# Performance work log

Hardware: AMD Instinct MI355X
Metric: run time of the kernel (lower is better)

Reference implementation:

```python
import jax, jax.numpy as jnp
import numpy as np

ITERATIONS = 3


def squash(s):
    # Faithful to the torch code: norm is taken over axis 2 (the labels axis
    # for s_j of shape (B, 1, L, O)), exactly as torch's squash(dim=2) does.
    mag_sq = jnp.sum(s * s, axis=2, keepdims=True)
    mag = jnp.sqrt(mag_sq)
    return mag_sq / (1.0 + mag_sq) * (s / mag)


def setup_inputs() -> dict:
    key = jax.random.key(0)
    kx, kw = jax.random.split(key)
    B, N, P, L, O = 256, 8, 1152, 10, 16
    x = jax.random.normal(kx, (B, N, P), dtype=jnp.float32)
    # nn.Parameter(torch.randn(1, P, L, O, N))
    W = jax.random.normal(kw, (1, P, L, O, N), dtype=jnp.float32)
    return {"x": x, "W": W}


def reference(x, W):
    # x: (B, N, P), W: (1, P, L, O, N)
    _, P, L, O, N = W.shape
    u = jnp.transpose(x, (0, 2, 1))  # (B, P, N)
    # u_hat[b,p,l,o] = sum_n W[0,p,l,o,n] * u[b,p,n]
    u_hat = jnp.einsum('plon,bpn->bplo', W[0], u)  # (B, P, L, O)

    b_ij = jnp.zeros((1, P, L, 1), dtype=u_hat.dtype)
    v_j = None
    for _ in range(ITERATIONS):
        # softmax over a size-1 trailing axis -> all ones (faithful to source)
        c_ij = jax.nn.softmax(b_ij, axis=-1)           # (1, P, L, 1)
        s_j = jnp.sum(c_ij * u_hat, axis=1, keepdims=True)  # (B, 1, L, O)
        v_j = squash(s_j)                               # (B, 1, L, O)
        # agreement: <u_hat, v_j> over output dim, then mean over batch
        agree = jnp.einsum('bplo,blo->bpl', u_hat, v_j[:, 0])  # (B, P, L)
        b_ij = b_ij + jnp.mean(agree, axis=0)[None, :, :, None]
    return jnp.squeeze(v_j)  # (B, L, O)
```

## Files before the change

### kernel.cpp

```cpp
#include <hip/hip_runtime.h>
#include <math.h>

#define B_TOT 256
#define N_N   8
#define P_P   1152
#define J_J   160
#define K_K   9216
#define L_L   10

#define SG 18
#define JG 5

typedef __attribute__((ext_vector_type(8))) short short8;
typedef __attribute__((ext_vector_type(4))) float f32x4;

__device__ __forceinline__ short f2bf(float f) {
    unsigned u = __builtin_bit_cast(unsigned, f);
    unsigned r = (u + 0x7fffu + ((u >> 16) & 1u)) >> 16;
    return (short)r;
}

__global__ __launch_bounds__(256) void gemm_direct(const float* __restrict__ x,
                                                   const float* __restrict__ W,
                                                   float* __restrict__ part) {
    const int bt = blockIdx.x;
    const int sg = blockIdx.y;
    const int jg = blockIdx.z;
    const int tid  = threadIdx.x;
    const int w    = tid >> 6;
    const int lane = tid & 63;
    const int b0 = bt * 16;
    const int p0 = sg * 64;
    const int j0 = jg * 32;

    __shared__ short As[16][520];
    __shared__ float redux[4][64][8];

    {
        const float* xb = x + (size_t)b0 * K_K + p0 + lane;
        #pragma unroll
        for (int i = 0; i < 4; ++i) {
            const int bb = w * 4 + i;
            const float* xr = xb + (size_t)bb * K_K;
            short8 sh;
            #pragma unroll
            for (int n = 0; n < 8; ++n)
                sh[n] = f2bf(xr[(size_t)n * P_P]);
            *reinterpret_cast<short8*>(&As[bb][lane * 8]) = sh;
        }
    }
    __syncthreads();

    const int m  = lane & 15;
    const int kq = lane >> 4;

    f32x4 acc0 = {0.f, 0.f, 0.f, 0.f};
    f32x4 acc1 = {0.f, 0.f, 0.f, 0.f};

    const float* wbase = W + (size_t)(p0 + w * 16 + kq) * 1280 + (size_t)(j0 + m) * 8;

    #pragma unroll
    for (int ks = 0; ks < 4; ++ks) {
        const short8 af =
            *reinterpret_cast<const short8*>(&As[m][w * 128 + ks * 32 + kq * 8]);
        const float* wp0 = wbase + (size_t)ks * 4 * 1280;
        const float* wp1 = wp0 + 128;
        const f32x4 a0 = *reinterpret_cast<const f32x4*>(wp0);
        const f32x4 a1 = *reinterpret_cast<const f32x4*>(wp0 + 4);
        const f32x4 c0 = *reinterpret_cast<const f32x4*>(wp1);
        const f32x4 c1 = *reinterpret_cast<const f32x4*>(wp1 + 4);
        short8 bf0, bf1;
        bf0[0] = f2bf(a0.x); bf0[1] = f2bf(a0.y); bf0[2] = f2bf(a0.z); bf0[3] = f2bf(a0.w);
        bf0[4] = f2bf(a1.x); bf0[5] = f2bf(a1.y); bf0[6] = f2bf(a1.z); bf0[7] = f2bf(a1.w);
        bf1[0] = f2bf(c0.x); bf1[1] = f2bf(c0.y); bf1[2] = f2bf(c0.z); bf1[3] = f2bf(c0.w);
        bf1[4] = f2bf(c1.x); bf1[5] = f2bf(c1.y); bf1[6] = f2bf(c1.z); bf1[7] = f2bf(c1.w);
        acc0 = __builtin_amdgcn_mfma_f32_16x16x32_bf16(af, bf0, acc0, 0, 0, 0);
        acc1 = __builtin_amdgcn_mfma_f32_16x16x32_bf16(af, bf1, acc1, 0, 0, 0);
    }

    #pragma unroll
    for (int r = 0; r < 4; ++r) {
        redux[w][lane][r]     = acc0[r];
        redux[w][lane][r + 4] = acc1[r];
    }
    __syncthreads();

    #pragma unroll
    for (int f = tid; f < 512; f += 256) {
        const int ln = f >> 3;
        const int c  = f & 7;
        const float s = redux[0][ln][c] + redux[1][ln][c]
                      + redux[2][ln][c] + redux[3][ln][c];
        const int mm = ln & 15;
        const int kk = ln >> 4;
        const int ch = c >> 2;
        const int r  = c & 3;
        const int b  = b0 + kk * 4 + r;
        const int j  = j0 + ch * 16 + mm;
        part[((size_t)b * SG + sg) * J_J + j] = s;
    }
}

__global__ __launch_bounds__(192) void reduce_squash(const float* __restrict__ part,
                                                     float* __restrict__ out) {
    const int b = blockIdx.x;
    const int j = threadIdx.x;
    __shared__ float sld[J_J];
    float s = 0.0f;
    if (j < J_J) {
        const float* pb = part + (size_t)b * SG * J_J + j;
        #pragma unroll 6
        for (int si = 0; si < SG; ++si)
            s += pb[(size_t)si * J_J];
        sld[j] = s;
    }
    __syncthreads();
    if (j < J_J) {
        const int o = j & 15;
        float msq = 0.0f;
        #pragma unroll
        for (int l = 0; l < L_L; ++l) {
            const float v = sld[l * 16 + o];
            msq = fmaf(v, v, msq);
        }
        const float mag = sqrtf(msq);
        out[(size_t)b * J_J + j] = s * (mag / (1.0f + msq));
    }
}

extern "C" void kernel_launch(void* const* d_in, const int* in_sizes, int n_in,
                              void* d_out, int out_size, void* d_ws, size_t ws_size,
                              hipStream_t stream) {
    const float* x = (const float*)d_in[0];
    const float* W = (const float*)d_in[1];
    float* out = (float*)d_out;

    float* part = (float*)d_ws;

    dim3 gg(B_TOT / 16, SG, JG);
    gemm_direct<<<gg, 256, 0, stream>>>(x, W, part);

    reduce_squash<<<B_TOT, 192, 0, stream>>>(part, out);
}
```

Baseline: 18.67 us.

## Double batch tile per block to reuse converted W fragments across two MFMA rows

Each block now covers 32 batch rows instead of 16, so every W fragment loaded from global memory and converted to bf16 feeds four MFMAs instead of two. This halves total W traffic and conversion work and halves the grid size. The reduction buffer is padded to 17 to limit LDS bank conflicts, and the bf16 conversion now uses the HIP intrinsic. In exchange there are fewer blocks (720) and more LDS and registers per block, which may reduce latency hiding.

```diff
diff --git a/kernel.cpp b/kernel.cpp
--- a/kernel.cpp
+++ b/kernel.cpp
@@ -1,4 +1,5 @@
 #include <hip/hip_runtime.h>
+#include <hip/hip_bf16.h>
 #include <math.h>
 
 #define B_TOT 256
@@ -15,9 +16,8 @@
 typedef __attribute__((ext_vector_type(4))) float f32x4;
 
 __device__ __forceinline__ short f2bf(float f) {
-    unsigned u = __builtin_bit_cast(unsigned, f);
-    unsigned r = (u + 0x7fffu + ((u >> 16) & 1u)) >> 16;
-    return (short)r;
+    __hip_bfloat16 h = __float2bfloat16(f);
+    return __builtin_bit_cast(short, h);
 }
 
 __global__ __launch_bounds__(256) void gemm_direct(const float* __restrict__ x,
@@ -29,40 +29,41 @@
     const int tid  = threadIdx.x;
     const int w    = tid >> 6;
     const int lane = tid & 63;
-    const int b0 = bt * 16;
+    const int b0 = bt * 32;
     const int p0 = sg * 64;
     const int j0 = jg * 32;
 
-    __shared__ short As[16][520];
-    __shared__ float redux[4][64][8];
+    __shared__ short As[32][520];
+    __shared__ float redux[4][64][17];
 
-    {
-        const float* xb = x + (size_t)b0 * K_K + p0 + lane;
+    #pragma unroll
+    for (int i = 0; i < 8; ++i) {
+        const int bb = w * 8 + i;
+        const float* xr = x + (size_t)(b0 + bb) * K_K + p0 + lane;
+        short8 sh;
         #pragma unroll
-        for (int i = 0; i < 4; ++i) {
-            const int bb = w * 4 + i;
-            const float* xr = xb + (size_t)bb * K_K;
-            short8 sh;
-            #pragma unroll
-            for (int n = 0; n < 8; ++n)
-                sh[n] = f2bf(xr[(size_t)n * P_P]);
-            *reinterpret_cast<short8*>(&As[bb][lane * 8]) = sh;
-        }
+        for (int n = 0; n < 8; ++n)
+            sh[n] = f2bf(xr[(size_t)n * P_P]);
+        *reinterpret_cast<short8*>(&As[bb][lane * 8]) = sh;
     }
     __syncthreads();
 
     const int m  = lane & 15;
     const int kq = lane >> 4;
 
-    f32x4 acc0 = {0.f, 0.f, 0.f, 0.f};
-    f32x4 acc1 = {0.f, 0.f, 0.f, 0.f};
+    f32x4 acc00 = {0.f, 0.f, 0.f, 0.f};
+    f32x4 acc01 = {0.f, 0.f, 0.f, 0.f};
+    f32x4 acc10 = {0.f, 0.f, 0.f, 0.f};
+    f32x4 acc11 = {0.f, 0.f, 0.f, 0.f};
 
     const float* wbase = W + (size_t)(p0 + w * 16 + kq) * 1280 + (size_t)(j0 + m) * 8;
 
     #pragma unroll
     for (int ks = 0; ks < 4; ++ks) {
-        const short8 af =
+        const short8 af0 =
             *reinterpret_cast<const short8*>(&As[m][w * 128 + ks * 32 + kq * 8]);
+        const short8 af1 =
+            *reinterpret_cast<const short8*>(&As[m + 16][w * 128 + ks * 32 + kq * 8]);
         const float* wp0 = wbase + (size_t)ks * 4 * 1280;
         const float* wp1 = wp0 + 128;
         const f32x4 a0 = *reinterpret_cast<const f32x4*>(wp0);
@@ -74,29 +75,34 @@
         bf0[4] = f2bf(a1.x); bf0[5] = f2bf(a1.y); bf0[6] = f2bf(a1.z); bf0[7] = f2bf(a1.w);
         bf1[0] = f2bf(c0.x); bf1[1] = f2bf(c0.y); bf1[2] = f2bf(c0.z); bf1[3] = f2bf(c0.w);
         bf1[4] = f2bf(c1.x); bf1[5] = f2bf(c1.y); bf1[6] = f2bf(c1.z); bf1[7] = f2bf(c1.w);
-        acc0 = __builtin_amdgcn_mfma_f32_16x16x32_bf16(af, bf0, acc0, 0, 0, 0);
-        acc1 = __builtin_amdgcn_mfma_f32_16x16x32_bf16(af, bf1, acc1, 0, 0, 0);
+        acc00 = __builtin_amdgcn_mfma_f32_16x16x32_bf16(af0, bf0, acc00, 0, 0, 0);
+        acc01 = __builtin_amdgcn_mfma_f32_16x16x32_bf16(af0, bf1, acc01, 0, 0, 0);
+        acc10 = __builtin_amdgcn_mfma_f32_16x16x32_bf16(af1, bf0, acc10, 0, 0, 0);
+        acc11 = __builtin_amdgcn_mfma_f32_16x16x32_bf16(af1, bf1, acc11, 0, 0, 0);
     }
 
     #pragma unroll
     for (int r = 0; r < 4; ++r) {
-        redux[w][lane][r]     = acc0[r];
-        redux[w][lane][r + 4] = acc1[r];
+        redux[w][lane][r]      = acc00[r];
+        redux[w][lane][r + 4]  = acc01[r];
+        redux[w][lane][r + 8]  = acc10[r];
+        redux[w][lane][r + 12] = acc11[r];
     }
     __syncthreads();
 
     #pragma unroll
-    for (int f = tid; f < 512; f += 256) {
-        const int ln = f >> 3;
-        const int c  = f & 7;
+    for (int f = tid; f < 1024; f += 256) {
+        const int ln = f >> 4;
+        const int c  = f & 15;
         const float s = redux[0][ln][c] + redux[1][ln][c]
                       + redux[2][ln][c] + redux[3][ln][c];
         const int mm = ln & 15;
         const int kk = ln >> 4;
-        const int ch = c >> 2;
+        const int bi = c >> 3;
+        const int ji = (c >> 2) & 1;
         const int r  = c & 3;
-        const int b  = b0 + kk * 4 + r;
-        const int j  = j0 + ch * 16 + mm;
+        const int b  = b0 + bi * 16 + kk * 4 + r;
+        const int j  = j0 + ji * 16 + mm;
         part[((size_t)b * SG + sg) * J_J + j] = s;
     }
 }
@@ -137,7 +143,7 @@
 
     float* part = (float*)d_ws;
 
-    dim3 gg(B_TOT / 16, SG, JG);
+    dim3 gg(B_TOT / 32, SG, JG);
     gemm_direct<<<gg, 256, 0, stream>>>(x, W, part);
 
     reduce_squash<<<B_TOT, 192, 0, stream>>>(part, out);
```

New measurement: 18.06 us. 3.3% less time.
